# Performance work log

Measured on AMD Instinct MI355X. Metric: run time of the kernel, lower is better.

## Reference

```python
import jax, jax.numpy as jnp
import numpy as np

K = 2  # kernel_size


def setup_inputs() -> dict:
    key = jax.random.key(0)
    x = jax.random.normal(key, (16, 64, 224, 224), dtype=jnp.float32)
    return {"x": x}


def reference(x):
    # Faithful translation of KernelActivation.forward.
    # NOTE: in the original torch code the per-patch activation results are
    # computed and then discarded; the returned tensor `repatched` is built
    # from `patches` alone, i.e. a pure element permutation of x:
    #   patches = x.unfold(1,k,k).unfold(2,k,k)      # (b, c//k, h//k, w, k, k)
    #   out = patches.contiguous().view(-1,1,k,k).reshape(-1, c, h, w)
    # torch unfold(1,k,k):  (b, c//k, h, w, k)   new dim appended for dim-1 slices
    # then unfold(2,k,k):   (b, c//k, h//k, w, k, k)
    # element (b,i,j,w,p,q) == x[b, i*k+p, j*k+q, w]
    k = K
    b, c, h, w = x.shape
    # reshape gives index order (b, i, p, j, q, w); transpose to (b, i, j, w, p, q)
    patches = x.reshape(b, c // k, k, h // k, k, w).transpose(0, 1, 3, 5, 2, 4)
    return patches.reshape(b, c, h, w)
```

## Files before the change

kernel.cpp:

```cpp
#include <hip/hip_runtime.h>


constexpr int Wd = 224;
constexpr int Hd = 224;
constexpr int Cd = 64;
constexpr int HW = Hd * Wd;
constexpr int HALF_H = Hd / 2;
constexpr int HALF_C = Cd / 2;

__global__ __launch_bounds__(256)
void permute_kernel(const float* __restrict__ x, float4* __restrict__ out, int n_groups) {
    int g = blockIdx.x * blockDim.x + threadIdx.x;
    if (g >= n_groups) return;

    int w = g % Wd;
    int t = g / Wd;
    int j = t % HALF_H;
    int u = t / HALF_H;
    int i = u % HALF_C;
    int b = u / HALF_C;

    const float* __restrict__ p = x + (((size_t)(b * Cd + 2 * i) * Hd + 2 * j) * Wd + w);
    float v00 = p[0];
    float v01 = p[Wd];
    float v10 = p[HW];
    float v11 = p[HW + Wd];

    out[g] = make_float4(v00, v01, v10, v11);
}

extern "C" void kernel_launch(void* const* d_in, const int* in_sizes, int n_in,
                              void* d_out, int out_size, void* d_ws, size_t ws_size,
                              hipStream_t stream) {
    const float* x = (const float*)d_in[0];
    float4* out = (float4*)d_out;

    int n_groups = out_size / 4;
    int block = 256;
    int grid = (n_groups + block - 1) / block;

    permute_kernel<<<grid, block, 0, stream>>>(x, out, n_groups);
}
```

Measured before the change: 325.6 us.

## Load float4 per thread and transpose 4x4 blocks with warp shuffles

Result: no change. 325.9 us (+0.1%).

```diff
diff --git a/kernel.cpp b/kernel.cpp
--- a/kernel.cpp
+++ b/kernel.cpp
@@ -1,43 +1,50 @@
 #include <hip/hip_runtime.h>
 
 
-constexpr int Wd = 224;
-constexpr int Hd = 224;
-constexpr int Cd = 64;
-constexpr int HW = Hd * Wd;
-constexpr int HALF_H = Hd / 2;
-constexpr int HALF_C = Cd / 2;
+constexpr int ROW4 = 224 / 4;
+constexpr int PLANE4 = 224 * 224 / 4;
 
 __global__ __launch_bounds__(256)
-void permute_kernel(const float* __restrict__ x, float4* __restrict__ out, int n_groups) {
-    int g = blockIdx.x * blockDim.x + threadIdx.x;
-    if (g >= n_groups) return;
+void permute_kernel(const float4* __restrict__ x4, float4* __restrict__ out) {
+    int gid = blockIdx.x * 256 + threadIdx.x;
+    int r = gid & 3;
+    int Q = gid >> 2;
 
-    int w = g % Wd;
-    int t = g / Wd;
-    int j = t % HALF_H;
-    int u = t / HALF_H;
-    int i = u % HALF_C;
-    int b = u / HALF_C;
+    int wq = Q % 56;
+    int t  = Q / 56;
+    int j  = t % 112;
+    int u  = t / 112;
+    int i  = u & 31;
+    int b  = u >> 5;
 
-    const float* __restrict__ p = x + (((size_t)(b * Cd + 2 * i) * Hd + 2 * j) * Wd + w);
-    float v00 = p[0];
-    float v01 = p[Wd];
-    float v10 = p[HW];
-    float v11 = p[HW + Wd];
+    int rc = r >> 1, rh = r & 1;
+    int src = (b * 64 + 2 * i + rc) * PLANE4 + (2 * j + rh) * ROW4 + wq;
+    float4 v = x4[src];
 
-    out[g] = make_float4(v00, v01, v10, v11);
+    float s0 = (r & 2) ? v.x : v.z;
+    float s1 = (r & 2) ? v.y : v.w;
+    s0 = __shfl_xor(s0, 2);
+    s1 = __shfl_xor(s1, 2);
+    if (r & 2) { v.x = s0; v.y = s1; } else { v.z = s0; v.w = s1; }
+
+    float t0 = (r & 1) ? v.x : v.y;
+    float t1 = (r & 1) ? v.z : v.w;
+    t0 = __shfl_xor(t0, 1);
+    t1 = __shfl_xor(t1, 1);
+    if (r & 1) { v.x = t0; v.z = t1; } else { v.y = t0; v.w = t1; }
+
+    out[gid] = v;
 }
 
 extern "C" void kernel_launch(void* const* d_in, const int* in_sizes, int n_in,
                               void* d_out, int out_size, void* d_ws, size_t ws_size,
                               hipStream_t stream) {
-    const float* x = (const float*)d_in[0];
+    const float4* x4 = (const float4*)d_in[0];
     float4* out = (float4*)d_out;
 
-    int n_groups = out_size / 4;
+    int n_threads = out_size / 4;
     int block = 256;
-    int grid = (n_groups + block - 1) / block;
+    int grid = n_threads / block;
 
-    permute_kernel<<<grid, block, 0, stream>>>(x, out, n_groups);
+    permute_kernel<<<grid, block, 0, stream>>>(x4, out);
 }
```
